# Kernel tuning notes

Measured on AMD Instinct MI355X. Metric: run time of the kernel, lower is better.

The kernel has to match this reference:

```python
import jax, jax.numpy as jnp
import numpy as np

B, T, J, C, H = 128, 512, 21, 3, 64


def setup_inputs() -> dict:
    key = jax.random.key(0)
    ks = jax.random.split(key, 14)
    x = jax.random.normal(ks[0], (B, T, J, C), dtype=jnp.float32)
    # Fixed skeleton-like adjacency buffer: symmetric, self-loops, row-normalized.
    A = (jax.random.uniform(ks[1], (J, J)) < 0.15).astype(jnp.float32)
    A = jnp.clip(A + A.T, 0.0, 1.0) + jnp.eye(J, dtype=jnp.float32)
    A = A / A.sum(axis=1, keepdims=True)
    s = 0.05
    W1 = jax.random.normal(ks[2], (H, C), jnp.float32) * s
    b1 = jnp.zeros((H,), jnp.float32)
    W2 = jax.random.normal(ks[3], (H, H), jnp.float32) * s
    b2 = jnp.zeros((H,), jnp.float32)
    Wa = jax.random.normal(ks[4], (1, H), jnp.float32) * s
    ba = jnp.zeros((1,), jnp.float32)
    W_ih = jax.random.normal(ks[5], (3 * H, J * H), jnp.float32) * s
    b_ih = jnp.zeros((3 * H,), jnp.float32)
    W_hh = jax.random.normal(ks[6], (3 * H, H), jnp.float32) * s
    b_hh = jnp.zeros((3 * H,), jnp.float32)
    W_head = jax.random.normal(ks[7], (J * C, H), jnp.float32) * s
    b_head = jnp.zeros((J * C,), jnp.float32)
    return {"x": x, "A": A, "W1": W1, "b1": b1, "W2": W2, "b2": b2,
            "Wa": Wa, "ba": ba, "W_ih": W_ih, "b_ih": b_ih,
            "W_hh": W_hh, "b_hh": b_hh, "W_head": W_head, "b_head": b_head}


def _gcn(A, x, W, b):
    # aggregated = einsum('ij,btjc->btic'); then Linear + ReLU
    agg = jnp.einsum('ij,btjc->btic', A, x)
    return jax.nn.relu(agg @ W.T + b)


def reference(x, A, W1, b1, W2, b2, Wa, ba, W_ih, b_ih, W_hh, b_hh, W_head, b_head):
    h = _gcn(A, x, W1, b1)            # (B,T,J,H)
    h = _gcn(A, h, W2, b2)            # (B,T,J,H)
    # Spatial attention: per-node score, mean over time, softmax over joints
    scores = (h @ Wa.T + ba).mean(axis=1)        # (B,J,1)
    attn = jax.nn.softmax(scores, axis=1)        # (B,J,1)
    h = h * attn[:, None]                        # (B,T,J,H)
    b_, t_, j_, c_ = h.shape
    seq = h.reshape(b_, t_, j_ * c_)             # (B,T,J*H)
    # GRU (PyTorch convention). Precompute input projections outside the scan.
    xproj = seq @ W_ih.T + b_ih                  # (B,T,3H)
    h0 = jnp.zeros((b_, H), xproj.dtype)

    def step(hprev, xp):
        gh = hprev @ W_hh.T + b_hh
        xr, xz, xn = jnp.split(xp, 3, axis=-1)
        hr, hz, hn = jnp.split(gh, 3, axis=-1)
        r = jax.nn.sigmoid(xr + hr)
        z = jax.nn.sigmoid(xz + hz)
        n = jnp.tanh(xn + r * hn)
        hnew = (1.0 - z) * n + z * hprev
        return hnew, None

    hT, _ = jax.lax.scan(step, h0, jnp.swapaxes(xproj, 0, 1))  # last hidden state
    out = hT @ W_head.T + b_head                 # (B, J*C)
    return out, attn.squeeze(-1)
```

## Files before the change

kernel.cpp:

```cpp
#include <hip/hip_runtime.h>
#include <cstdint>
#include <cstddef>

#define NB 128
#define NT 512
#define NJ 21
#define NC 3
#define NH 64
#define JH 1344
#define G3 192
#define OUT0 (NB*NJ*NC)
#define FB 4

typedef __attribute__((ext_vector_type(8))) __bf16 bf16x8;
typedef __attribute__((ext_vector_type(4))) float f32x4;

__device__ __forceinline__ float bf2f(unsigned short u) {
  union { unsigned int i; float f; } v; v.i = ((unsigned int)u) << 16; return v.f;
}
__device__ __forceinline__ unsigned short f2bf(float f) {
  union { float f; unsigned int i; } v; v.f = f;
  unsigned int x = v.i;
  unsigned int lsb = (x >> 16) & 1u;
  x += 0x7fffu + lsb;
  return (unsigned short)(x >> 16);
}
__device__ __forceinline__ unsigned int pk_bf16(float lo, float hi) {
  unsigned int r;
  asm("v_cvt_pk_bf16_f32 %0, %1, %2" : "=v"(r) : "v"(lo), "v"(hi));
  return r;
}
__device__ __forceinline__ unsigned int scale2(unsigned int u, float s) {
  float lo = __uint_as_float(u << 16);
  float hi = __uint_as_float(u & 0xffff0000u);
  return pk_bf16(lo * s, hi * s);
}

__global__ __launch_bounds__(256) void k0_convw(
    const float* __restrict__ W, unsigned short* __restrict__ Wbf) {
  const int ti = blockIdx.x*256 + threadIdx.x;
  const float4 v = ((const float4*)W)[ti];
  uint2 o;
  o.x = (unsigned int)f2bf(v.x) | ((unsigned int)f2bf(v.y) << 16);
  o.y = (unsigned int)f2bf(v.z) | ((unsigned int)f2bf(v.w) << 16);
  ((uint2*)Wbf)[ti] = o;
}

__global__ __launch_bounds__(256, 2) void k1_fused(
    const float* __restrict__ x, const float* __restrict__ A,
    const float* __restrict__ W1, const float* __restrict__ b1,
    const float* __restrict__ W2, const float* __restrict__ b2,
    const float* __restrict__ Wa,
    unsigned short* __restrict__ h2out, float* __restrict__ scorepart) {
  __shared__ unsigned short h1s[FB*32*72];
  __shared__ unsigned short us[FB*64*40];
  __shared__ unsigned short w2s[64*72];
  __shared__ unsigned short adjs[32*40];
  __shared__ unsigned short h2st[FB*NJ*72];
  __shared__ float afs[NJ*NJ];
  __shared__ float xs[4][64];
  __shared__ float ags[4][64];
  __shared__ float spred[4][NJ];

  const int tid = threadIdx.x;
  const int w = tid >> 6, l = tid & 63;
  const int q = l >> 4, r = l & 15;
  const int b = blockIdx.x >> 7, ch = blockIdx.x & 127;
  const int t0 = ch * FB;

  for (int i = tid; i < NJ*NJ; i += 256) afs[i] = A[i];
  for (int i = tid; i < 1024; i += 256) {
    const int ii = i >> 5, jj = i & 31;
    adjs[ii*40 + jj] = (ii < NJ && jj < NJ) ? f2bf(A[ii*NJ + jj]) : (unsigned short)0;
  }
  {
    const int h = tid & 63, qd = tid >> 6;
    const int g0 = qd * 16;
#pragma unroll
    for (int e = 0; e < 16; e += 2) {
      const float v0 = W2[h*64 + g0 + e], v1 = W2[h*64 + g0 + e + 1];
      ((unsigned int*)w2s)[h*36 + ((g0 + e) >> 1)] = pk_bf16(v0, v1);
    }
  }
#pragma unroll
  for (int j = NJ; j < 32; ++j)
    ((unsigned int*)h1s)[(w*32 + j)*36 + (l & 31)] = 0u;

  const float w1r0 = W1[l*3+0], w1r1 = W1[l*3+1], w1r2 = W1[l*3+2];
  const float b1h = b1[l];
  float b2v[4][4], wav[4][4];
#pragma unroll
  for (int mt = 0; mt < 4; ++mt)
#pragma unroll
    for (int rg = 0; rg < 4; ++rg) {
      const int h = mt*16 + q*4 + rg;
      b2v[mt][rg] = b2[h]; wav[mt][rg] = Wa[h];
    }
  __syncthreads();

  {
    const size_t fr = (size_t)(b*NT + t0 + w);
    if (l < NJ*NC) xs[w][l] = x[fr*(NJ*NC) + l];
    if (l < NJ*NC) {
      const int ji = l / 3, c = l - ji*3;
      float s = 0.f;
#pragma unroll
      for (int j = 0; j < NJ; ++j) s += afs[ji*NJ + j] * xs[w][j*3 + c];
      ags[w][l] = s;
    }
#pragma unroll
    for (int j = 0; j < NJ; ++j) {
      float v = b1h + w1r0*ags[w][j*3+0] + w1r1*ags[w][j*3+1] + w1r2*ags[w][j*3+2];
      v = fmaxf(v, 0.f);
      h1s[(w*32 + j)*72 + l] = f2bf(v);
    }
  }
  __syncthreads();

  bf16x8 bw[2][4];
#pragma unroll
  for (int ks = 0; ks < 2; ++ks)
#pragma unroll
    for (int nt = 0; nt < 4; ++nt)
      bw[ks][nt] = *(const bf16x8*)(&w2s[(nt*16 + r)*72 + (ks*4 + q)*8]);
  f32x4 acc1[2][4];
#pragma unroll
  for (int i = 0; i < 2; ++i)
#pragma unroll
    for (int j2 = 0; j2 < 4; ++j2) acc1[i][j2] = (f32x4)0.f;
#pragma unroll
  for (int mti = 0; mti < 2; ++mti) {
    const int row = (w*2 + mti)*16 + r;
#pragma unroll
    for (int ks = 0; ks < 2; ++ks) {
      const bf16x8 af = *(const bf16x8*)(&h1s[row*72 + (ks*4 + q)*8]);
#pragma unroll
      for (int nt = 0; nt < 4; ++nt)
        acc1[mti][nt] = __builtin_amdgcn_mfma_f32_16x16x32_bf16(af, bw[ks][nt], acc1[mti][nt], 0,0,0);
    }
  }
#pragma unroll
  for (int mti = 0; mti < 2; ++mti)
#pragma unroll
    for (int nt = 0; nt < 4; ++nt) {
      const int h = nt*16 + r;
#pragma unroll
      for (int rp = 0; rp < 2; ++rp) {
        const int jp = mti*16 + q*4 + rp*2;
        ((unsigned int*)us)[(w*64 + h)*20 + (jp >> 1)] =
            pk_bf16(acc1[mti][nt][rp*2], acc1[mti][nt][rp*2+1]);
      }
    }
  __syncthreads();

  bf16x8 badj[2];
#pragma unroll
  for (int nt = 0; nt < 2; ++nt)
    badj[nt] = *(const bf16x8*)(&adjs[(nt*16 + r)*40 + q*8]);
  f32x4 acc2[4][2];
#pragma unroll
  for (int i = 0; i < 4; ++i) { acc2[i][0] = (f32x4)0.f; acc2[i][1] = (f32x4)0.f; }
#pragma unroll
  for (int mt = 0; mt < 4; ++mt) {
    const int h = mt*16 + r;
    const bf16x8 af = *(const bf16x8*)(&us[(w*64 + h)*40 + q*8]);
#pragma unroll
    for (int nt = 0; nt < 2; ++nt)
      acc2[mt][nt] = __builtin_amdgcn_mfma_f32_16x16x32_bf16(af, badj[nt], acc2[mt][nt], 0,0,0);
  }
  float sp0 = 0.f, sp1 = 0.f;
#pragma unroll
  for (int nt = 0; nt < 2; ++nt) {
    const int i = nt*16 + r;
    if (i < NJ) {
#pragma unroll
      for (int mt = 0; mt < 4; ++mt)
#pragma unroll
        for (int rp = 0; rp < 2; ++rp) {
          const int h0 = mt*16 + q*4 + rp*2;
          const float v0 = fmaxf(acc2[mt][nt][rp*2]   + b2v[mt][rp*2],   0.f);
          const float v1 = fmaxf(acc2[mt][nt][rp*2+1] + b2v[mt][rp*2+1], 0.f);
          if (nt == 0) sp0 += v0*wav[mt][rp*2] + v1*wav[mt][rp*2+1];
          else         sp1 += v0*wav[mt][rp*2] + v1*wav[mt][rp*2+1];
          ((unsigned int*)h2st)[(w*NJ + i)*36 + (h0 >> 1)] = pk_bf16(v0, v1);
        }
    }
  }
  sp0 += __shfl_xor(sp0, 16); sp0 += __shfl_xor(sp0, 32);
  sp1 += __shfl_xor(sp1, 16); sp1 += __shfl_xor(sp1, 32);
  if (l < 16) spred[w][l] = sp0;
  if (l < 5)  spred[w][16 + l] = sp1;
  __syncthreads();

  if (tid < NJ)
    scorepart[((size_t)b*128 + ch)*NJ + tid] =
      spred[0][tid] + spred[1][tid] + spred[2][tid] + spred[3][tid];

  const size_t gbase = (size_t)(b*NT + t0) * JH;
  for (int cid = tid; cid < FB*NJ*8; cid += 256) {
    const int f = cid / (NJ*8), rem = cid - f*(NJ*8);
    const int i = rem >> 3, p = rem & 7;
    const uint4 v = *(const uint4*)(&h2st[(f*NJ + i)*72 + p*8]);
    *(uint4*)(&h2out[gbase + (size_t)f*JH + i*64 + p*8]) = v;
  }
}

__global__ __launch_bounds__(64) void k2_attn(
    const float* __restrict__ scorepart, float* __restrict__ attn,
    float* __restrict__ out_attn) {
  __shared__ float ss[NJ];
  const int b = blockIdx.x, tid = threadIdx.x;
  if (tid < NJ) {
    float s = 0.f;
    for (int ch = 0; ch < 128; ++ch) s += scorepart[(b*128 + ch)*NJ + tid];
    ss[tid] = s * (1.0f/NT);
  }
  __syncthreads();
  float m = -1e30f;
  for (int j = 0; j < NJ; ++j) m = fmaxf(m, ss[j]);
  float sum = 0.f;
  for (int j = 0; j < NJ; ++j) sum += expf(ss[j] - m);
  if (tid < NJ) {
    float a = expf(ss[tid] - m) / sum;
    attn[b*NJ + tid] = a;
    out_attn[b*NJ + tid] = a;
  }
}

__global__ __launch_bounds__(256, 2) void k3_xproj_mfma(
    const unsigned short* __restrict__ h2, const unsigned short* __restrict__ Wbf,
    const float* __restrict__ b_ih, const float* __restrict__ attn,
    float* __restrict__ xproj) {
  __shared__ unsigned short Abuf[2][128*32];
  __shared__ unsigned short Bbuf[2][192*32];
  const int tid = threadIdx.x;
  const int w = tid >> 6, l = tid & 63;
  const int lq = l >> 4, lr = l & 15;
  const int blk = blockIdx.x;
  const int b = blk >> 2;
  const int t0 = (blk & 3) << 7;
  const int wm = w >> 1, wn = w & 1;

  const unsigned short* gA[2]; int ldsA[2];
#pragma unroll
  for (int i = 0; i < 2; ++i) {
    const int lc = tid*2 + i, rr = lc >> 2, j = lc & 3;
    gA[i] = h2 + (size_t)(b*NT + t0 + rr)*JH + j*8;
    ldsA[i] = rr*32 + ((j ^ ((rr>>1)&3)) << 3);
  }
  const unsigned short* gB[3]; int ldsB[3];
#pragma unroll
  for (int i = 0; i < 3; ++i) {
    const int lc = tid + 256*i, g = lc >> 2, j = lc & 3;
    gB[i] = Wbf + (size_t)g*JH + j*8;
    ldsB[i] = g*32 + ((j ^ ((g>>1)&3)) << 3);
  }
  int aoff[4], boff[6];
#pragma unroll
  for (int mt = 0; mt < 4; ++mt) {
    const int row = wm*64 + mt*16 + lr;
    aoff[mt] = row*32 + ((lq ^ ((row>>1)&3)) << 3);
  }
#pragma unroll
  for (int nt = 0; nt < 6; ++nt) {
    const int g = wn*96 + nt*16 + lr;
    boff[nt] = g*32 + ((lq ^ ((g>>1)&3)) << 3);
  }

  f32x4 acc[4][6];
#pragma unroll
  for (int mt = 0; mt < 4; ++mt)
#pragma unroll
    for (int nt = 0; nt < 6; ++nt) acc[mt][nt] = (f32x4)0.f;

  {
    const float s = attn[b*NJ + 0];
#pragma unroll
    for (int i = 0; i < 2; ++i)
      *(uint4*)(&Abuf[0][ldsA[i]]) = *(const uint4*)(gA[i]);
#pragma unroll
    for (int i = 0; i < 3; ++i) {
      uint4 v = *(const uint4*)(gB[i]);
      v.x = scale2(v.x, s); v.y = scale2(v.y, s);
      v.z = scale2(v.z, s); v.w = scale2(v.w, s);
      *(uint4*)(&Bbuf[0][ldsB[i]]) = v;
    }
  }
  __syncthreads();

  for (int ks = 0; ks < 42; ++ks) {
    const int cur = ks & 1;
    uint4 av0, av1, bv0, bv1, bv2;
    if (ks < 41) {
      const int kk = (ks+1)*32;
      av0 = *(const uint4*)(gA[0] + kk);
      av1 = *(const uint4*)(gA[1] + kk);
      bv0 = *(const uint4*)(gB[0] + kk);
      bv1 = *(const uint4*)(gB[1] + kk);
      bv2 = *(const uint4*)(gB[2] + kk);
    }
    bf16x8 af[4], bfr[6];
#pragma unroll
    for (int mt = 0; mt < 4; ++mt) af[mt] = *(const bf16x8*)(&Abuf[cur][aoff[mt]]);
#pragma unroll
    for (int nt = 0; nt < 6; ++nt) bfr[nt] = *(const bf16x8*)(&Bbuf[cur][boff[nt]]);
#pragma unroll
    for (int mt = 0; mt < 4; ++mt)
#pragma unroll
      for (int nt = 0; nt < 6; ++nt)
        acc[mt][nt] = __builtin_amdgcn_mfma_f32_16x16x32_bf16(af[mt], bfr[nt], acc[mt][nt], 0, 0, 0);
    if (ks < 41) {
      const float s = attn[b*NJ + ((ks+1) >> 1)];
      *(uint4*)(&Abuf[cur^1][ldsA[0]]) = av0;
      *(uint4*)(&Abuf[cur^1][ldsA[1]]) = av1;
      uint4 v;
      v = bv0; v.x = scale2(v.x, s); v.y = scale2(v.y, s); v.z = scale2(v.z, s); v.w = scale2(v.w, s);
      *(uint4*)(&Bbuf[cur^1][ldsB[0]]) = v;
      v = bv1; v.x = scale2(v.x, s); v.y = scale2(v.y, s); v.z = scale2(v.z, s); v.w = scale2(v.w, s);
      *(uint4*)(&Bbuf[cur^1][ldsB[1]]) = v;
      v = bv2; v.x = scale2(v.x, s); v.y = scale2(v.y, s); v.z = scale2(v.z, s); v.w = scale2(v.w, s);
      *(uint4*)(&Bbuf[cur^1][ldsB[2]]) = v;
    }
    __syncthreads();
  }

  float bias[6];
#pragma unroll
  for (int nt = 0; nt < 6; ++nt) bias[nt] = b_ih[wn*96 + nt*16 + lr];
#pragma unroll
  for (int mt = 0; mt < 4; ++mt)
#pragma unroll
    for (int nt = 0; nt < 6; ++nt) {
      const int g = wn*96 + nt*16 + lr;
#pragma unroll
      for (int rr = 0; rr < 4; ++rr) {
        const int trow = t0 + wm*64 + mt*16 + lq*4 + rr;
        xproj[(size_t)(b*NT + trow)*G3 + g] = acc[mt][nt][rr] + bias[nt];
      }
    }
}

__global__ __launch_bounds__(192) void k4_gru(
    const float* __restrict__ xproj, const float* __restrict__ W_hh,
    const float* __restrict__ b_hh, float* __restrict__ hT) {
  __shared__ float h_s[2][NH];
  __shared__ float rz_s[2*NH];
  __shared__ float xn_s[NH];
  __shared__ float hn_s[NH];
  const int b = blockIdx.x, g = threadIdx.x;
  float wh[NH];
  {
    const float4* p = (const float4*)(W_hh + g*NH);
#pragma unroll
    for (int qq = 0; qq < 16; ++qq) {
      float4 v = p[qq];
      wh[4*qq+0]=v.x; wh[4*qq+1]=v.y; wh[4*qq+2]=v.z; wh[4*qq+3]=v.w;
    }
  }
  const float bh = b_hh[g];
  if (g < NH) h_s[0][g] = 0.f;
  __syncthreads();
  int cur = 0;
  const float* xp_base = xproj + (size_t)b*NT*G3;
  float xp = xp_base[g];
  for (int t = 0; t < NT; ++t) {
    float xp_next = (t+1 < NT) ? xp_base[(size_t)(t+1)*G3 + g] : 0.f;
    float a0=0.f, a1=0.f, a2=0.f, a3=0.f;
    const float4* h4 = (const float4*)(h_s[cur]);
#pragma unroll
    for (int qq = 0; qq < 16; qq += 4) {
      float4 v0 = h4[qq+0], v1 = h4[qq+1], v2 = h4[qq+2], v3 = h4[qq+3];
      a0 += v0.x*wh[4*qq+0]  + v0.y*wh[4*qq+1]  + v0.z*wh[4*qq+2]  + v0.w*wh[4*qq+3];
      a1 += v1.x*wh[4*qq+4]  + v1.y*wh[4*qq+5]  + v1.z*wh[4*qq+6]  + v1.w*wh[4*qq+7];
      a2 += v2.x*wh[4*qq+8]  + v2.y*wh[4*qq+9]  + v2.z*wh[4*qq+10] + v2.w*wh[4*qq+11];
      a3 += v3.x*wh[4*qq+12] + v3.y*wh[4*qq+13] + v3.z*wh[4*qq+14] + v3.w*wh[4*qq+15];
    }
    const float gh = bh + ((a0 + a1) + (a2 + a3));
    if (g < 2*NH) { rz_s[g] = xp + gh; }
    else          { xn_s[g-2*NH] = xp; hn_s[g-2*NH] = gh; }
    __syncthreads();
    if (g < NH) {
      const float r = 1.f/(1.f + expf(-rz_s[g]));
      const float z = 1.f/(1.f + expf(-rz_s[NH+g]));
      const float n = tanhf(xn_s[g] + r*hn_s[g]);
      h_s[cur^1][g] = (1.f - z)*n + z*h_s[cur][g];
    }
    __syncthreads();
    cur ^= 1;
    xp = xp_next;
  }
  if (g < NH) hT[b*NH + g] = h_s[cur][g];
}

__global__ __launch_bounds__(256) void k5_head(
    const float* __restrict__ hT, const float* __restrict__ W_head,
    const float* __restrict__ b_head, float* __restrict__ out) {
  const int idx = blockIdx.x*256 + threadIdx.x;
  if (idx >= NB*63) return;
  const int b = idx / 63, rr = idx % 63;
  const float* hv = hT + b*NH;
  const float* wr = W_head + rr*NH;
  float acc = b_head[rr];
#pragma unroll
  for (int k = 0; k < NH; ++k) acc += hv[k]*wr[k];
  out[idx] = acc;
}

extern "C" void kernel_launch(void* const* d_in, const int* in_sizes, int n_in,
                              void* d_out, int out_size, void* d_ws, size_t ws_size,
                              hipStream_t stream) {
  const float* x      = (const float*)d_in[0];
  const float* A      = (const float*)d_in[1];
  const float* W1     = (const float*)d_in[2];
  const float* b1     = (const float*)d_in[3];
  const float* W2     = (const float*)d_in[4];
  const float* b2     = (const float*)d_in[5];
  const float* Wa     = (const float*)d_in[6];
  const float* W_ih   = (const float*)d_in[8];
  const float* b_ih   = (const float*)d_in[9];
  const float* W_hh   = (const float*)d_in[10];
  const float* b_hh   = (const float*)d_in[11];
  const float* W_head = (const float*)d_in[12];
  const float* b_head = (const float*)d_in[13];
  float* out = (float*)d_out;

  char* ws = (char*)d_ws;
  size_t off = 0;
  unsigned short* h2 = (unsigned short*)(ws + off); off += (size_t)NB*NT*JH*2;
  float* scorepart   = (float*)(ws + off);          off += (size_t)NB*128*NJ*4;
  float* attn        = (float*)(ws + off);          off += (size_t)NB*NJ*4;
  off = (off + 15) & ~(size_t)15;
  float* xproj       = (float*)(ws + off);          off += (size_t)NB*NT*G3*4;
  float* hT          = (float*)(ws + off);          off += (size_t)NB*NH*4;
  off = (off + 15) & ~(size_t)15;
  unsigned short* Wbf = (unsigned short*)(ws + off); off += (size_t)G3*JH*2;

  k0_convw<<<dim3(252),       256, 0, stream>>>(W_ih, Wbf);
  k1_fused<<<dim3(NB*128),    256, 0, stream>>>(x, A, W1, b1, W2, b2, Wa, h2, scorepart);
  k2_attn<<<dim3(NB),          64, 0, stream>>>(scorepart, attn, out + OUT0);
  k3_xproj_mfma<<<dim3(512),  256, 0, stream>>>(h2, Wbf, b_ih, attn, xproj);
  k4_gru <<<dim3(NB),         192, 0, stream>>>(xproj, W_hh, b_hh, hT);
  k5_head<<<dim3((NB*63 + 255)/256), 256, 0, stream>>>(hT, W_head, b_head, out);
}
```

Before: 555.6 us.

## Run GRU recurrence in a single wavefront with per-thread three-gate compute

```diff
diff --git a/kernel.cpp b/kernel.cpp
--- a/kernel.cpp
+++ b/kernel.cpp
@@ -340,56 +340,71 @@
     }
 }
 
-__global__ __launch_bounds__(192) void k4_gru(
+__global__ __launch_bounds__(64, 1) void k4_gru_wave(
     const float* __restrict__ xproj, const float* __restrict__ W_hh,
     const float* __restrict__ b_hh, float* __restrict__ hT) {
-  __shared__ float h_s[2][NH];
-  __shared__ float rz_s[2*NH];
-  __shared__ float xn_s[NH];
-  __shared__ float hn_s[NH];
+  __shared__ __align__(16) float hs[NH];
   const int b = blockIdx.x, g = threadIdx.x;
-  float wh[NH];
+
+  float wr[NH], wz[NH], wn[NH];
   {
-    const float4* p = (const float4*)(W_hh + g*NH);
-#pragma unroll
-    for (int qq = 0; qq < 16; ++qq) {
-      float4 v = p[qq];
-      wh[4*qq+0]=v.x; wh[4*qq+1]=v.y; wh[4*qq+2]=v.z; wh[4*qq+3]=v.w;
-    }
-  }
-  const float bh = b_hh[g];
-  if (g < NH) h_s[0][g] = 0.f;
-  __syncthreads();
-  int cur = 0;
-  const float* xp_base = xproj + (size_t)b*NT*G3;
-  float xp = xp_base[g];
-  for (int t = 0; t < NT; ++t) {
-    float xp_next = (t+1 < NT) ? xp_base[(size_t)(t+1)*G3 + g] : 0.f;
-    float a0=0.f, a1=0.f, a2=0.f, a3=0.f;
-    const float4* h4 = (const float4*)(h_s[cur]);
-#pragma unroll
-    for (int qq = 0; qq < 16; qq += 4) {
-      float4 v0 = h4[qq+0], v1 = h4[qq+1], v2 = h4[qq+2], v3 = h4[qq+3];
-      a0 += v0.x*wh[4*qq+0]  + v0.y*wh[4*qq+1]  + v0.z*wh[4*qq+2]  + v0.w*wh[4*qq+3];
-      a1 += v1.x*wh[4*qq+4]  + v1.y*wh[4*qq+5]  + v1.z*wh[4*qq+6]  + v1.w*wh[4*qq+7];
-      a2 += v2.x*wh[4*qq+8]  + v2.y*wh[4*qq+9]  + v2.z*wh[4*qq+10] + v2.w*wh[4*qq+11];
-      a3 += v3.x*wh[4*qq+12] + v3.y*wh[4*qq+13] + v3.z*wh[4*qq+14] + v3.w*wh[4*qq+15];
-    }
-    const float gh = bh + ((a0 + a1) + (a2 + a3));
-    if (g < 2*NH) { rz_s[g] = xp + gh; }
-    else          { xn_s[g-2*NH] = xp; hn_s[g-2*NH] = gh; }
-    __syncthreads();
-    if (g < NH) {
-      const float r = 1.f/(1.f + expf(-rz_s[g]));
-      const float z = 1.f/(1.f + expf(-rz_s[NH+g]));
-      const float n = tanhf(xn_s[g] + r*hn_s[g]);
-      h_s[cur^1][g] = (1.f - z)*n + z*h_s[cur][g];
-    }
-    __syncthreads();
-    cur ^= 1;
-    xp = xp_next;
-  }
-  if (g < NH) hT[b*NH + g] = h_s[cur][g];
+    const float4* pr = (const float4*)(W_hh + (size_t)g*NH);
+    const float4* pz = (const float4*)(W_hh + (size_t)(NH + g)*NH);
+    const float4* pn = (const float4*)(W_hh + (size_t)(2*NH + g)*NH);
+#pragma unroll
+    for (int q = 0; q < 16; ++q) {
+      const float4 vr = pr[q], vz = pz[q], vn = pn[q];
+      wr[4*q+0]=vr.x; wr[4*q+1]=vr.y; wr[4*q+2]=vr.z; wr[4*q+3]=vr.w;
+      wz[4*q+0]=vz.x; wz[4*q+1]=vz.y; wz[4*q+2]=vz.z; wz[4*q+3]=vz.w;
+      wn[4*q+0]=vn.x; wn[4*q+1]=vn.y; wn[4*q+2]=vn.z; wn[4*q+3]=vn.w;
+    }
+  }
+  const float br = b_hh[g], bz = b_hh[NH + g], bn = b_hh[2*NH + g];
+  const float* xb = xproj + (size_t)b*NT*G3;
+
+  hs[g] = 0.f;
+  float hprev = 0.f;
+  float pxr[4], pxz[4], pxn[4];
+#pragma unroll
+  for (int p = 0; p < 4; ++p) {
+    pxr[p] = xb[(size_t)p*G3 + g] + br;
+    pxz[p] = xb[(size_t)p*G3 + NH + g] + bz;
+    pxn[p] = xb[(size_t)p*G3 + 2*NH + g] + bn;
+  }
+  __syncthreads();
+
+  for (int t = 0; t < NT; t += 4) {
+#pragma unroll
+    for (int p = 0; p < 4; ++p) {
+      int tf = t + 4 + p; if (tf >= NT) tf = NT - 1;
+      const float nxr = xb[(size_t)tf*G3 + g];
+      const float nxz = xb[(size_t)tf*G3 + NH + g];
+      const float nxn = xb[(size_t)tf*G3 + 2*NH + g];
+
+      float ar0=0.f, ar1=0.f, az0=0.f, az1=0.f, an0=0.f, an1=0.f;
+      const float4* h4 = (const float4*)hs;
+#pragma unroll
+      for (int q = 0; q < 16; q += 2) {
+        const float4 v0 = h4[q], v1 = h4[q+1];
+        ar0 += v0.x*wr[4*q+0] + v0.y*wr[4*q+1] + v0.z*wr[4*q+2] + v0.w*wr[4*q+3];
+        az0 += v0.x*wz[4*q+0] + v0.y*wz[4*q+1] + v0.z*wz[4*q+2] + v0.w*wz[4*q+3];
+        an0 += v0.x*wn[4*q+0] + v0.y*wn[4*q+1] + v0.z*wn[4*q+2] + v0.w*wn[4*q+3];
+        ar1 += v1.x*wr[4*q+4] + v1.y*wr[4*q+5] + v1.z*wr[4*q+6] + v1.w*wr[4*q+7];
+        az1 += v1.x*wz[4*q+4] + v1.y*wz[4*q+5] + v1.z*wz[4*q+6] + v1.w*wz[4*q+7];
+        an1 += v1.x*wn[4*q+4] + v1.y*wn[4*q+5] + v1.z*wn[4*q+6] + v1.w*wn[4*q+7];
+      }
+      const float hr = ar0 + ar1, hz = az0 + az1, hn = an0 + an1;
+      const float rr = 1.f/(1.f + __expf(-(pxr[p] + hr)));
+      const float zz = 1.f/(1.f + __expf(-(pxz[p] + hz)));
+      const float nx = pxn[p] + rr*hn;
+      const float nn = 2.f/(1.f + __expf(-2.f*nx)) - 1.f;
+      hprev = (1.f - zz)*nn + zz*hprev;
+      hs[g] = hprev;
+      __syncthreads();
+      pxr[p] = nxr + br; pxz[p] = nxz + bz; pxn[p] = nxn + bn;
+    }
+  }
+  hT[b*NH + g] = hprev;
 }
 
 __global__ __launch_bounds__(256) void k5_head(
@@ -439,6 +454,6 @@
   k1_fused<<<dim3(NB*128),    256, 0, stream>>>(x, A, W1, b1, W2, b2, Wa, h2, scorepart);
   k2_attn<<<dim3(NB),          64, 0, stream>>>(scorepart, attn, out + OUT0);
   k3_xproj_mfma<<<dim3(512),  256, 0, stream>>>(h2, Wbf, b_ih, attn, xproj);
-  k4_gru <<<dim3(NB),         192, 0, stream>>>(xproj, W_hh, b_hh, hT);
+  k4_gru_wave<<<dim3(NB),      64, 0, stream>>>(xproj, W_hh, b_hh, hT);
   k5_head<<<dim3((NB*63 + 255)/256), 256, 0, stream>>>(hT, W_head, b_head, out);
 }
```

Result: slower. 620.8 us (+11.7%).

## Batch GRU recurrence across 16 sequences with bf16 MFMA and split precision

Applied to the files above, without the earlier changes.

```diff
diff --git a/kernel.cpp b/kernel.cpp
--- a/kernel.cpp
+++ b/kernel.cpp
@@ -332,64 +332,114 @@
 #pragma unroll
     for (int nt = 0; nt < 6; ++nt) {
       const int g = wn*96 + nt*16 + lr;
-#pragma unroll
-      for (int rr = 0; rr < 4; ++rr) {
-        const int trow = t0 + wm*64 + mt*16 + lq*4 + rr;
-        xproj[(size_t)(b*NT + trow)*G3 + g] = acc[mt][nt][rr] + bias[nt];
-      }
-    }
-}
-
-__global__ __launch_bounds__(192) void k4_gru(
+      const int trow = t0 + wm*64 + mt*16 + lq*4;
+      float4 o;
+      o.x = acc[mt][nt][0] + bias[nt];
+      o.y = acc[mt][nt][1] + bias[nt];
+      o.z = acc[mt][nt][2] + bias[nt];
+      o.w = acc[mt][nt][3] + bias[nt];
+      *(float4*)(&xproj[(size_t)(b*G3 + g)*NT + trow]) = o;
+    }
+}
+
+__global__ __launch_bounds__(512, 1) void k4_gru_mfma(
     const float* __restrict__ xproj, const float* __restrict__ W_hh,
     const float* __restrict__ b_hh, float* __restrict__ hT) {
-  __shared__ float h_s[2][NH];
-  __shared__ float rz_s[2*NH];
-  __shared__ float xn_s[NH];
-  __shared__ float hn_s[NH];
-  const int b = blockIdx.x, g = threadIdx.x;
-  float wh[NH];
-  {
-    const float4* p = (const float4*)(W_hh + g*NH);
-#pragma unroll
-    for (int qq = 0; qq < 16; ++qq) {
-      float4 v = p[qq];
-      wh[4*qq+0]=v.x; wh[4*qq+1]=v.y; wh[4*qq+2]=v.z; wh[4*qq+3]=v.w;
-    }
-  }
-  const float bh = b_hh[g];
-  if (g < NH) h_s[0][g] = 0.f;
-  __syncthreads();
-  int cur = 0;
-  const float* xp_base = xproj + (size_t)b*NT*G3;
-  float xp = xp_base[g];
-  for (int t = 0; t < NT; ++t) {
-    float xp_next = (t+1 < NT) ? xp_base[(size_t)(t+1)*G3 + g] : 0.f;
-    float a0=0.f, a1=0.f, a2=0.f, a3=0.f;
-    const float4* h4 = (const float4*)(h_s[cur]);
-#pragma unroll
-    for (int qq = 0; qq < 16; qq += 4) {
-      float4 v0 = h4[qq+0], v1 = h4[qq+1], v2 = h4[qq+2], v3 = h4[qq+3];
-      a0 += v0.x*wh[4*qq+0]  + v0.y*wh[4*qq+1]  + v0.z*wh[4*qq+2]  + v0.w*wh[4*qq+3];
-      a1 += v1.x*wh[4*qq+4]  + v1.y*wh[4*qq+5]  + v1.z*wh[4*qq+6]  + v1.w*wh[4*qq+7];
-      a2 += v2.x*wh[4*qq+8]  + v2.y*wh[4*qq+9]  + v2.z*wh[4*qq+10] + v2.w*wh[4*qq+11];
-      a3 += v3.x*wh[4*qq+12] + v3.y*wh[4*qq+13] + v3.z*wh[4*qq+14] + v3.w*wh[4*qq+15];
-    }
-    const float gh = bh + ((a0 + a1) + (a2 + a3));
-    if (g < 2*NH) { rz_s[g] = xp + gh; }
-    else          { xn_s[g-2*NH] = xp; hn_s[g-2*NH] = gh; }
-    __syncthreads();
-    if (g < NH) {
-      const float r = 1.f/(1.f + expf(-rz_s[g]));
-      const float z = 1.f/(1.f + expf(-rz_s[NH+g]));
-      const float n = tanhf(xn_s[g] + r*hn_s[g]);
-      h_s[cur^1][g] = (1.f - z)*n + z*h_s[cur][g];
-    }
-    __syncthreads();
-    cur ^= 1;
-    xp = xp_next;
-  }
-  if (g < NH) hT[b*NH + g] = h_s[cur][g];
+  __shared__ __align__(16) unsigned short hb[2][2][16*72];
+  const int tid = threadIdx.x;
+  const int w = tid >> 6, l = tid & 63, q = l >> 4, r15 = l & 15;
+  const int b0 = blockIdx.x * 16;
+
+  for (int i = tid; i < 2*2*16*72; i += 512) (&hb[0][0][0])[i] = 0;
+
+  bf16x8 afr[2][2];
+  int chv[2]; float br_[2], bz_[2], bn_[2];
+#pragma unroll
+  for (int i = 0; i < 2; ++i) {
+    const int mt = 2*w + i;
+    const int row = mt*16 + r15;
+    const int chs = row >> 2, gate = row & 3;
+#pragma unroll
+    for (int ks = 0; ks < 2; ++ks) {
+      union { bf16x8 v; unsigned int u[4]; } tu;
+      if (gate < 3) {
+        const float* src = W_hh + (size_t)(gate*NH + chs)*NH + ks*32 + q*8;
+        const float4 a = *(const float4*)(src);
+        const float4 b = *(const float4*)(src + 4);
+        tu.u[0] = pk_bf16(a.x, a.y); tu.u[1] = pk_bf16(a.z, a.w);
+        tu.u[2] = pk_bf16(b.x, b.y); tu.u[3] = pk_bf16(b.z, b.w);
+      } else {
+        tu.u[0]=0u; tu.u[1]=0u; tu.u[2]=0u; tu.u[3]=0u;
+      }
+      afr[i][ks] = tu.v;
+    }
+    chv[i] = mt*4 + q;
+    br_[i] = b_hh[chv[i]]; bz_[i] = b_hh[NH + chv[i]]; bn_[i] = b_hh[2*NH + chv[i]];
+  }
+
+  const float* xrow[2][3];
+#pragma unroll
+  for (int i = 0; i < 2; ++i)
+#pragma unroll
+    for (int e = 0; e < 3; ++e)
+      xrow[i][e] = xproj + (size_t)((b0 + r15)*G3 + e*NH + chv[i]) * NT;
+
+  f32x4 cur[2][3], nxt[2][3];
+#pragma unroll
+  for (int i = 0; i < 2; ++i)
+#pragma unroll
+    for (int e = 0; e < 3; ++e) cur[i][e] = *(const f32x4*)(xrow[i][e]);
+
+  float hprev[2] = {0.f, 0.f};
+  __syncthreads();
+
+  for (int tg = 0; tg < NT; tg += 4) {
+    if (tg + 4 < NT) {
+#pragma unroll
+      for (int i = 0; i < 2; ++i)
+#pragma unroll
+        for (int e = 0; e < 3; ++e) nxt[i][e] = *(const f32x4*)(xrow[i][e] + tg + 4);
+    }
+#pragma unroll
+    for (int p = 0; p < 4; ++p) {
+      const int rb = p & 1, wb = rb ^ 1;
+      const bf16x8 bhi0 = *(const bf16x8*)(&hb[rb][0][r15*72 + q*8]);
+      const bf16x8 bhi1 = *(const bf16x8*)(&hb[rb][0][r15*72 + 32 + q*8]);
+      const bf16x8 blo0 = *(const bf16x8*)(&hb[rb][1][r15*72 + q*8]);
+      const bf16x8 blo1 = *(const bf16x8*)(&hb[rb][1][r15*72 + 32 + q*8]);
+#pragma unroll
+      for (int i = 0; i < 2; ++i) {
+        f32x4 acc = (f32x4)0.f;
+        acc = __builtin_amdgcn_mfma_f32_16x16x32_bf16(afr[i][0], blo0, acc, 0,0,0);
+        acc = __builtin_amdgcn_mfma_f32_16x16x32_bf16(afr[i][1], blo1, acc, 0,0,0);
+        acc = __builtin_amdgcn_mfma_f32_16x16x32_bf16(afr[i][0], bhi0, acc, 0,0,0);
+        acc = __builtin_amdgcn_mfma_f32_16x16x32_bf16(afr[i][1], bhi1, acc, 0,0,0);
+        const float xr = cur[i][0][p], xz = cur[i][1][p], xn = cur[i][2][p];
+        const float hr = acc[0] + br_[i];
+        const float hz = acc[1] + bz_[i];
+        const float hn = acc[2] + bn_[i];
+        const float rr = __builtin_amdgcn_rcpf(1.f + __expf(-(xr + hr)));
+        const float zz = __builtin_amdgcn_rcpf(1.f + __expf(-(xz + hz)));
+        const float nx = xn + rr*hn;
+        const float nn = 2.f*__builtin_amdgcn_rcpf(1.f + __expf(-2.f*nx)) - 1.f;
+        const float h = (1.f - zz)*nn + zz*hprev[i];
+        hprev[i] = h;
+        const unsigned short hi16 = f2bf(h);
+        const unsigned short lo16 = f2bf(h - bf2f(hi16));
+        hb[wb][0][r15*72 + chv[i]] = hi16;
+        hb[wb][1][r15*72 + chv[i]] = lo16;
+      }
+      __syncthreads();
+    }
+#pragma unroll
+    for (int i = 0; i < 2; ++i)
+#pragma unroll
+      for (int e = 0; e < 3; ++e) cur[i][e] = nxt[i][e];
+  }
+
+#pragma unroll
+  for (int i = 0; i < 2; ++i)
+    hT[(size_t)(b0 + r15)*NH + chv[i]] = hprev[i];
 }
 
 __global__ __launch_bounds__(256) void k5_head(
@@ -439,6 +489,6 @@
   k1_fused<<<dim3(NB*128),    256, 0, stream>>>(x, A, W1, b1, W2, b2, Wa, h2, scorepart);
   k2_attn<<<dim3(NB),          64, 0, stream>>>(scorepart, attn, out + OUT0);
   k3_xproj_mfma<<<dim3(512),  256, 0, stream>>>(h2, Wbf, b_ih, attn, xproj);
-  k4_gru <<<dim3(NB),         192, 0, stream>>>(xproj, W_hh, b_hh, hT);
+  k4_gru_mfma<<<dim3(8),      512, 0, stream>>>(xproj, W_hh, b_hh, hT);
   k5_head<<<dim3((NB*63 + 255)/256), 256, 0, stream>>>(hT, W_head, b_head, out);
 }
```

After: 605.0 us. 1.09x slower.
